# Kernel optimization log

Hardware: AMD Instinct MI355X
Metric: run time of the kernel (lower is better)

The kernel has to match this reference:

```python
import jax, jax.numpy as jnp
import numpy as np
from jax import lax

V = 33      # n_vertices
EPS = 1e-5  # instance-norm eps


def _resize_bilinear(x, oh, ow):
    # torch F.interpolate bilinear, align_corners=False, antialias=False
    b, c, H, W = x.shape
    def coords(out, size):
        src = (jnp.arange(out, dtype=jnp.float32) + 0.5) * (size / out) - 0.5
        i0 = jnp.clip(jnp.floor(src).astype(jnp.int32), 0, size - 1)
        i1 = jnp.clip(i0 + 1, 0, size - 1)
        f = jnp.clip(src - i0.astype(jnp.float32), 0.0, 1.0)
        return i0, i1, f
    y0, y1, fy = coords(oh, H)
    x0, x1, fx = coords(ow, W)
    rows = x[:, :, y0, :] * (1 - fy)[None, None, :, None] + x[:, :, y1, :] * fy[None, None, :, None]
    return rows[:, :, :, x0] * (1 - fx) + rows[:, :, :, x1] * fx


def _conv_s2(x, w, b):
    y = lax.conv_general_dilated(x, w, (2, 2), [(1, 1), (1, 1)],
                                 dimension_numbers=('NCHW', 'OIHW', 'NCHW'))
    return y + b[None, :, None, None]


def _lrelu(x):
    return jnp.where(x >= 0, x, 0.2 * x)


def _inorm(x, g, be):
    m = x.mean((2, 3), keepdims=True)
    v = x.var((2, 3), keepdims=True)
    return (x - m) / jnp.sqrt(v + EPS) * g[None, :, None, None] + be[None, :, None, None]


def _ailut_transform(imgs, luts, vertices):
    # imgs (b,3,H,W); luts (b,3,V,V,V) indexed [out_c, ib, ig, ir]; vertices (b,3,V)
    b, c, H, W = imgs.shape
    N = H * W
    x = jnp.clip(imgs, 0.0, 1.0).reshape(b, 3, N)
    ss = jax.vmap(jax.vmap(lambda v, q: jnp.searchsorted(v, q, side='right')))
    idx = jnp.clip(ss(vertices, x) - 1, 0, V - 2)            # (b,3,N)
    v0 = jnp.take_along_axis(vertices, idx, axis=-1)
    v1 = jnp.take_along_axis(vertices, idx + 1, axis=-1)
    frac = jnp.clip((x - v0) / jnp.maximum(v1 - v0, 1e-10), 0.0, 1.0)
    ir, ig, ibl = idx[:, 0], idx[:, 1], idx[:, 2]            # (b,N) each
    fr, fg, fb = frac[:, 0], frac[:, 1], frac[:, 2]
    lut_flat = luts.reshape(b, 3, V * V * V)
    out = jnp.zeros((b, 3, N), imgs.dtype)
    for db in (0, 1):
        wb = fb if db else 1.0 - fb
        for dg in (0, 1):
            wg = fg if dg else 1.0 - fg
            for dr in (0, 1):
                w = wb * wg * (fr if dr else 1.0 - fr)       # (b,N)
                flat = ((ibl + db) * V + (ig + dg)) * V + (ir + dr)
                vals = jnp.take_along_axis(lut_flat, jnp.broadcast_to(flat[:, None, :], (b, 3, N)), axis=-1)
                out = out + w[:, None, :] * vals
    return out.reshape(b, 3, H, W)


def setup_inputs() -> dict:
    key = jax.random.key(0)
    ks = jax.random.split(key, 32)
    n = lambda k, s: jax.random.normal(k, s, jnp.float32) * 0.05
    inp = {'imgs': jax.random.uniform(ks[0], (2, 3, 2048, 2048), jnp.float32)}
    chans = [(3, 16), (16, 32), (32, 64), (64, 128), (128, 128)]
    for i, (ci, co) in enumerate(chans, start=1):
        inp[f'w{i}'] = n(ks[2 * i], (co, ci, 3, 3))
        inp[f'b{i}'] = n(ks[2 * i + 1], (co,))
        if i <= 4:
            inp[f'g{i}'] = jnp.ones((co,), jnp.float32)
            inp[f'be{i}'] = jnp.zeros((co,), jnp.float32)
    inp['wgen_w'] = n(ks[12], (512, 3))
    inp['wgen_b'] = n(ks[13], (3,))
    inp['basis_w'] = n(ks[14], (3, 3 * V ** 3))
    inp['ada_w'] = n(ks[15], (512, 3 * (V - 1)))
    inp['ada_b'] = n(ks[16], (3 * (V - 1),))
    return inp


def reference(imgs, w1, b1, g1, be1, w2, b2, g2, be2, w3, b3, g3, be3,
              w4, b4, g4, be4, w5, b5, wgen_w, wgen_b, basis_w, ada_w, ada_b):
    b = imgs.shape[0]
    x = _resize_bilinear(imgs, 256, 256)
    for (w, bb, g, be) in ((w1, b1, g1, be1), (w2, b2, g2, be2),
                           (w3, b3, g3, be3), (w4, b4, g4, be4)):
        x = _inorm(_lrelu(_conv_s2(x, w, bb)), g, be)
    x = _lrelu(_conv_s2(x, w5, b5))                      # (b,128,8,8); dropout is identity at eval
    x = x.reshape(b, 128, 2, 4, 2, 4).mean((3, 5)).reshape(b, 512)  # AdaptiveAvgPool2d(2)
    weights = x @ wgen_w + wgen_b                        # (b,3) rank weights
    luts = (weights @ basis_w).reshape(b, 3, V, V, V)
    intervals = jax.nn.softmax((x @ ada_w + ada_b).reshape(b, 3, V - 1), axis=-1)
    vertices = jnp.pad(jnp.cumsum(intervals, -1), ((0, 0), (0, 0), (1, 0)))  # (b,3,V)
    return _ailut_transform(imgs, luts, vertices)
```

## Files before the change

### kernel.cpp

```cpp
#include <hip/hip_runtime.h>
#include <hip/hip_fp16.h>
#include <cstdint>
#include <cstddef>

#define VCUBE 35937
#define LUT_CH 107811

__global__ __launch_bounds__(256) void conv1_fused(const float* __restrict__ imgs,
    const float* __restrict__ w, const float* __restrict__ bias,
    float* __restrict__ out) {
  __shared__ float s_in[3*3*34];
  __shared__ float s_w[16*3*9];
  int bid = blockIdx.x;
  int owt = bid & 7; int oh = (bid >> 3) & 127; int b = bid >> 10;
  int t = threadIdx.x;
  int ow0 = owt * 16;
  int iwbase = 2*ow0 - 1;
  int ihbase = 2*oh - 1;
  for (int i = t; i < 3*3*34; i += 256) {
    int x = i % 34; int rest = i / 34; int kh = rest % 3; int ci = rest / 3;
    int ih = ihbase + kh;
    int iw = iwbase + x;
    float v = 0.f;
    if (ih >= 0 && ih < 256 && iw >= 0 && iw < 256) {
      const float* p = imgs + (size_t)(b*3+ci) * 2048 * 2048;
      int y0 = ih*8 + 3, x0 = iw*8 + 3;
      const float* r0 = p + (size_t)y0*2048 + x0;
      const float* r1 = r0 + 2048;
      float a = r0[0], bb = r0[1], c = r1[0], d = r1[1];
      float top = a + 0.5f*(bb - a);
      float bot = c + 0.5f*(d - c);
      v = top + 0.5f*(bot - top);
    }
    s_in[i] = v;
  }
  for (int i = t; i < 16*3*9; i += 256) s_w[i] = w[i];
  __syncthreads();
  int owl = t & 15; int co = t >> 4;
  float acc = bias[co];
  const float* wp = s_w + co*27;
#pragma unroll
  for (int ci = 0; ci < 3; ci++) {
#pragma unroll
    for (int kh = 0; kh < 3; kh++) {
      const float* rp = s_in + (ci*3 + kh)*34 + 2*owl;
      acc = fmaf(rp[0], wp[ci*9 + kh*3 + 0], acc);
      acc = fmaf(rp[1], wp[ci*9 + kh*3 + 1], acc);
      acc = fmaf(rp[2], wp[ci*9 + kh*3 + 2], acc);
    }
  }
  acc = acc >= 0.f ? acc : 0.2f*acc;
  out[(((size_t)b*16 + co)*128 + oh)*128 + ow0 + owl] = acc;
}

template<int CI, int CO, int IS, int COPB, bool WLDS>
__global__ __launch_bounds__(256) void conv_row(const float* __restrict__ in,
    const float* __restrict__ w, const float* __restrict__ bias,
    float* __restrict__ out) {
  constexpr int OS = IS/2;
  constexpr int PW = IS + 2;
  constexpr int NG = CO/COPB;
  constexpr int E  = CI*3*PW;
  static_assert(COPB*OS == 256, "block mismatch");
  __shared__ float s_in[E];
  __shared__ float s_w[WLDS ? COPB*CI*9 : 1];
  int bid = blockIdx.x;
  int grp = bid % NG; int rest = bid / NG; int oh = rest % OS; int b = rest / OS;
  int t = threadIdx.x;
  int ihb = 2*oh - 1;
  for (int i = t; i < E; i += 256) {
    int x = i % PW; int r2 = i / PW; int kh = r2 % 3; int ci = r2 / 3;
    int ih = ihb + kh; int iw = x - 1;
    float v = 0.f;
    if (ih >= 0 && ih < IS && iw >= 0 && iw < IS)
      v = in[((size_t)(b*CI + ci)*IS + ih)*IS + iw];
    s_in[i] = v;
  }
  if (WLDS) {
    const float* wg = w + (size_t)grp*COPB*CI*9;
    for (int i = t; i < COPB*CI*9; i += 256) s_w[i] = wg[i];
  }
  __syncthreads();
  int ow = t % OS; int col = t / OS;
  int co = grp*COPB + col;
  float acc = bias[co];
  const float* wp = WLDS ? (s_w + col*CI*9) : (w + (size_t)co*CI*9);
  for (int ci = 0; ci < CI; ci++) {
    const float* rowp = s_in + ci*3*PW;
    const float* wc = wp + ci*9;
#pragma unroll
    for (int kh = 0; kh < 3; kh++) {
      const float* rp = rowp + kh*PW + 2*ow;
      acc = fmaf(rp[0], wc[kh*3 + 0], acc);
      acc = fmaf(rp[1], wc[kh*3 + 1], acc);
      acc = fmaf(rp[2], wc[kh*3 + 2], acc);
    }
  }
  acc = acc >= 0.f ? acc : 0.2f*acc;
  out[(((size_t)b*CO + co)*OS + oh)*OS + ow] = acc;
}

__global__ __launch_bounds__(256) void inorm_kernel(float* __restrict__ x,
    const float* __restrict__ g, const float* __restrict__ be, int C, int HW) {
  int plane = blockIdx.x;
  int c = plane % C;
  float* p = x + (size_t)plane * HW;
  int t = threadIdx.x;
  float s = 0.f, s2 = 0.f;
  for (int i = t; i < HW; i += 256) {
    float v = p[i];
    s += v;
    s2 = fmaf(v, v, s2);
  }
  __shared__ float ss[256], sq[256];
  ss[t] = s; sq[t] = s2;
  __syncthreads();
  for (int off = 128; off > 0; off >>= 1) {
    if (t < off) { ss[t] += ss[t + off]; sq[t] += sq[t + off]; }
    __syncthreads();
  }
  __shared__ float sc, sh;
  if (t == 0) {
    float inv_n = 1.0f / (float)HW;
    float mean = ss[0] * inv_n;
    float var  = sq[0] * inv_n - mean*mean;
    float scale = g[c] / sqrtf(var + 1e-5f);
    sc = scale;
    sh = be[c] - mean*scale;
  }
  __syncthreads();
  for (int i = t; i < HW; i += 256) p[i] = fmaf(p[i], sc, sh);
}

__global__ __launch_bounds__(128) void head_kernel(const float* __restrict__ x5,
    const float* __restrict__ wgen_w, const float* __restrict__ wgen_b,
    const float* __restrict__ ada_w, const float* __restrict__ ada_b,
    float* __restrict__ gweights, float* __restrict__ vertices,
    float* __restrict__ invtab, uint8_t* __restrict__ hints) {
  int b = blockIdx.x; int t = threadIdx.x;
  __shared__ float xv[512];
  __shared__ float logits[96];
  __shared__ float svp[99];
  for (int o = t; o < 512; o += 128) {
    int c = o >> 2; int h2 = (o >> 1) & 1; int w2 = o & 1;
    const float* p = x5 + ((size_t)(b*128 + c))*64 + h2*32 + w2*4;
    float s = 0.f;
#pragma unroll
    for (int h = 0; h < 4; h++)
#pragma unroll
      for (int ww = 0; ww < 4; ww++) s += p[h*8 + ww];
    xv[o] = s * (1.f/16.f);
  }
  __syncthreads();
  if (t < 96) {
    float s = ada_b[t];
    for (int k = 0; k < 512; k++) s = fmaf(xv[k], ada_w[k*96 + t], s);
    logits[t] = s;
  } else if (t < 99) {
    int j = t - 96;
    float s = wgen_b[j];
    for (int k = 0; k < 512; k++) s = fmaf(xv[k], wgen_w[k*3 + j], s);
    gweights[b*3 + j] = s;
  }
  __syncthreads();
  if (t < 3) {
    const float* l = logits + t*32;
    float m = l[0];
#pragma unroll
    for (int i = 1; i < 32; i++) m = fmaxf(m, l[i]);
    float e[32]; float sum = 0.f;
#pragma unroll
    for (int i = 0; i < 32; i++) { e[i] = expf(l[i] - m); sum += e[i]; }
    float inv = 1.0f / sum;
    float* vp = vertices + b*99 + t*33;
    svp[t*33] = 0.f; vp[0] = 0.f;
    float cum = 0.f;
#pragma unroll
    for (int i = 0; i < 32; i++) { cum = fmaf(e[i], inv, cum); svp[t*33 + i + 1] = cum; vp[i + 1] = cum; }
  }
  __syncthreads();
  if (t < 96) {
    int c = t >> 5, i = t & 31;
    float d = svp[c*33 + i + 1] - svp[c*33 + i];
    invtab[b*96 + t] = 1.0f / fmaxf(d, 1e-10f);
  }
  for (int e = t; e < 3072; e += 128) {
    int c = e >> 10; int bin = e & 1023;
    float q0 = (float)bin * (1.f/1024.f);
    const float* v = svp + c*33;
    int lo = 0, hi = 33;
    while (lo < hi) { int mid = (lo + hi) >> 1; if (v[mid] <= q0) lo = mid + 1; else hi = mid; }
    int idx = lo - 1; if (idx > 31) idx = 31;
    hints[b*3072 + e] = (uint8_t)idx;
  }
}

__global__ __launch_bounds__(256) void ecell_build(const float* __restrict__ basis_w,
    const float* __restrict__ gw, __half* __restrict__ ecell, int B) {
  int tid = blockIdx.x*256 + threadIdx.x;
  int total = B * 32768 * 3;
  if (tid >= total) return;
  int cc = tid % 3;
  int cell = tid / 3;
  int r = cell & 31; int g = (cell >> 5) & 31; int bl = (cell >> 10) & 31; int b = cell >> 15;
  float w0 = gw[b*3 + 0], w1 = gw[b*3 + 1], w2 = gw[b*3 + 2];
  union { __half h[8]; uint4 u; } pk;
#pragma unroll
  for (int dbl = 0; dbl < 2; dbl++)
#pragma unroll
    for (int dg = 0; dg < 2; dg++)
#pragma unroll
      for (int dr = 0; dr < 2; dr++) {
        int flat = cc*VCUBE + ((bl + dbl)*33 + (g + dg))*33 + (r + dr);
        float val = w0*basis_w[flat] + w1*basis_w[LUT_CH + flat] + w2*basis_w[2*LUT_CH + flat];
        pk.h[dbl*4 + dg*2 + dr] = __float2half(val);
      }
  *(uint4*)((uint16_t*)ecell + (size_t)cell*32 + cc*8) = pk.u;
}

__device__ __forceinline__ void lut_px(float R, float G, float Bl,
    const __half* __restrict__ ec, const float* sv, const float* sinv,
    const uint8_t* shint, float* o0, float* o1, float* o2) {
  float q[3] = { fminf(fmaxf(R, 0.f), 1.f), fminf(fmaxf(G, 0.f), 1.f), fminf(fmaxf(Bl, 0.f), 1.f) };
  int id[3]; float fr[3];
#pragma unroll
  for (int c = 0; c < 3; c++) {
    float qc = q[c];
    int bin = (int)(qc * 1024.f); bin = bin > 1023 ? 1023 : bin;
    int idx = shint[(c << 10) + bin];
    const float* v = sv + c*33;
#pragma unroll
    for (int it = 0; it < 3; it++)
      idx += (idx < 31 && v[idx + 1] <= qc) ? 1 : 0;
    float f = (qc - v[idx]) * sinv[(c << 5) + idx];
    fr[c] = fminf(fmaxf(f, 0.f), 1.f);
    id[c] = idx;
  }
  const __half* cell = ec + ((size_t)(((id[2] << 5) + id[1]) << 5) + id[0]) * 32;
  float fR = fr[0], fG = fr[1], fB = fr[2];
  float res[3];
#pragma unroll
  for (int cc = 0; cc < 3; cc++) {
    uint4 u = *(const uint4*)(cell + cc*8);
    const __half* h = (const __half*)&u;
    float f0 = __half2float(h[0]), f1 = __half2float(h[1]);
    float f2 = __half2float(h[2]), f3 = __half2float(h[3]);
    float f4 = __half2float(h[4]), f5 = __half2float(h[5]);
    float f6 = __half2float(h[6]), f7 = __half2float(h[7]);
    float l00 = fmaf(fR, f1 - f0, f0);
    float l01 = fmaf(fR, f3 - f2, f2);
    float L0  = fmaf(fG, l01 - l00, l00);
    float l10 = fmaf(fR, f5 - f4, f4);
    float l11 = fmaf(fR, f7 - f6, f6);
    float L1  = fmaf(fG, l11 - l10, l10);
    res[cc] = fmaf(fB, L1 - L0, L0);
  }
  *o0 = res[0]; *o1 = res[1]; *o2 = res[2];
}

__global__ __launch_bounds__(256) void transform_kernel(const float* __restrict__ imgs,
    const __half* __restrict__ ecell, const float* __restrict__ vert,
    const float* __restrict__ invtab, const unsigned int* __restrict__ hintw,
    float* __restrict__ out, int B) {
  const size_t N = 2048u*2048u;
  __shared__ float sv[99];
  __shared__ float sinv[96];
  __shared__ unsigned int shint_w[768];
  int b = blockIdx.x % B;
  int pblk = blockIdx.x / B;
  int t = threadIdx.x;
  if (t < 99) sv[t] = vert[b*99 + t];
  if (t < 96) sinv[t] = invtab[b*96 + t];
  for (int i = t; i < 768; i += 256) shint_w[i] = hintw[b*768 + i];
  __syncthreads();
  const uint8_t* shint = (const uint8_t*)shint_w;
  size_t pix = ((size_t)pblk*256 + t) * 4;
  const float* ip = imgs + (size_t)b*3*N;
  float* op = out + (size_t)b*3*N;
  const __half* ec = ecell + (size_t)b*1048576;
  float4 r  = *(const float4*)(ip + pix);
  float4 g  = *(const float4*)(ip + N + pix);
  float4 bb = *(const float4*)(ip + 2*N + pix);
  float4 o0, o1, o2;
  lut_px(r.x, g.x, bb.x, ec, sv, sinv, shint, &o0.x, &o1.x, &o2.x);
  lut_px(r.y, g.y, bb.y, ec, sv, sinv, shint, &o0.y, &o1.y, &o2.y);
  lut_px(r.z, g.z, bb.z, ec, sv, sinv, shint, &o0.z, &o1.z, &o2.z);
  lut_px(r.w, g.w, bb.w, ec, sv, sinv, shint, &o0.w, &o1.w, &o2.w);
  *(float4*)(op + pix) = o0;
  *(float4*)(op + N + pix) = o1;
  *(float4*)(op + 2*N + pix) = o2;
}

extern "C" void kernel_launch(void* const* d_in, const int* in_sizes, int n_in,
                              void* d_out, int out_size, void* d_ws, size_t ws_size,
                              hipStream_t stream) {
  const float* imgs = (const float*)d_in[0];
  const float* w1 = (const float*)d_in[1];  const float* b1 = (const float*)d_in[2];
  const float* g1 = (const float*)d_in[3];  const float* be1 = (const float*)d_in[4];
  const float* w2 = (const float*)d_in[5];  const float* b2 = (const float*)d_in[6];
  const float* g2 = (const float*)d_in[7];  const float* be2 = (const float*)d_in[8];
  const float* w3 = (const float*)d_in[9];  const float* b3 = (const float*)d_in[10];
  const float* g3 = (const float*)d_in[11]; const float* be3 = (const float*)d_in[12];
  const float* w4 = (const float*)d_in[13]; const float* b4 = (const float*)d_in[14];
  const float* g4 = (const float*)d_in[15]; const float* be4 = (const float*)d_in[16];
  const float* w5 = (const float*)d_in[17]; const float* b5 = (const float*)d_in[18];
  const float* wgen_w  = (const float*)d_in[19];
  const float* wgen_b  = (const float*)d_in[20];
  const float* basis_w = (const float*)d_in[21];
  const float* ada_w   = (const float*)d_in[22];
  const float* ada_b   = (const float*)d_in[23];
  float* out = (float*)d_out;

  const int B = in_sizes[0] / (3*2048*2048);

  char* wsb = (char*)d_ws;
  __half* ecell = (__half*)wsb;
  size_t A_bytes = (size_t)B * 2097152;
  float* x1 = (float*)wsb;
  float* x2 = x1 + (size_t)B*262144;
  float* x3 = x2 + (size_t)B*131072;
  float* x4 = x3 + (size_t)B*65536;
  float* x5 = x4 + (size_t)B*32768;
  float* tail = (float*)(wsb + A_bytes);
  float* gw   = tail;
  float* vert = gw + (size_t)B*4;
  float* invt = vert + (size_t)B*99;
  uint8_t* hints = (uint8_t*)(invt + (size_t)B*96);

  conv1_fused<<<B*1024, 256, 0, stream>>>(imgs, w1, b1, x1);
  inorm_kernel<<<B*16, 256, 0, stream>>>(x1, g1, be1, 16, 128*128);
  conv_row<16, 32, 128, 4, true><<<B*512, 256, 0, stream>>>(x1, w2, b2, x2);
  inorm_kernel<<<B*32, 256, 0, stream>>>(x2, g2, be2, 32, 64*64);
  conv_row<32, 64, 64, 8, true><<<B*256, 256, 0, stream>>>(x2, w3, b3, x3);
  inorm_kernel<<<B*64, 256, 0, stream>>>(x3, g3, be3, 64, 32*32);
  conv_row<64, 128, 32, 16, true><<<B*128, 256, 0, stream>>>(x3, w4, b4, x4);
  inorm_kernel<<<B*128, 256, 0, stream>>>(x4, g4, be4, 128, 16*16);
  conv_row<128, 128, 16, 32, false><<<B*32, 256, 0, stream>>>(x4, w5, b5, x5);
  head_kernel<<<B, 128, 0, stream>>>(x5, wgen_w, wgen_b, ada_w, ada_b, gw, vert, invt, hints);
  ecell_build<<<B*384, 256, 0, stream>>>(basis_w, gw, ecell, B);
  transform_kernel<<<B*4096, 256, 0, stream>>>(imgs, ecell, vert, invt,
                                               (const unsigned int*)hints, out, B);
}
```

Before: 487.3 us.

## Fuse encoder, head and LUT build into persistent kernel with grid barriers

Replaces the chain of conv, instance-norm, head and ecell kernels with one persistent kernel of 128*B blocks that synchronises stages through atomic-counter grid barriers. Instance-norm statistics are accumulated with atomics in the conv epilogues and the normalisation is applied while loading the next layer's input, which removes the separate norm passes. The transform kernel also changes: it uses nontemporal loads and stores, batches the LUT gathers, interpolates in half2 arithmetic, and does one fewer search refinement step. The single kernel saves launch gaps but relies on every block being co-resident for the spin barriers, and the early encoder stages now run on fewer blocks. The half2 math and shorter search may also lower accuracy.

Result: slower. 707.0 us (+45.1%).

```diff
diff --git a/kernel.cpp b/kernel.cpp
--- a/kernel.cpp
+++ b/kernel.cpp
@@ -6,289 +6,455 @@
 #define VCUBE 35937
 #define LUT_CH 107811
 
-__global__ __launch_bounds__(256) void conv1_fused(const float* __restrict__ imgs,
-    const float* __restrict__ w, const float* __restrict__ bias,
-    float* __restrict__ out) {
-  __shared__ float s_in[3*3*34];
-  __shared__ float s_w[16*3*9];
-  int bid = blockIdx.x;
-  int owt = bid & 7; int oh = (bid >> 3) & 127; int b = bid >> 10;
-  int t = threadIdx.x;
-  int ow0 = owt * 16;
-  int iwbase = 2*ow0 - 1;
-  int ihbase = 2*oh - 1;
-  for (int i = t; i < 3*3*34; i += 256) {
-    int x = i % 34; int rest = i / 34; int kh = rest % 3; int ci = rest / 3;
-    int ih = ihbase + kh;
-    int iw = iwbase + x;
-    float v = 0.f;
-    if (ih >= 0 && ih < 256 && iw >= 0 && iw < 256) {
-      const float* p = imgs + (size_t)(b*3+ci) * 2048 * 2048;
-      int y0 = ih*8 + 3, x0 = iw*8 + 3;
-      const float* r0 = p + (size_t)y0*2048 + x0;
-      const float* r1 = r0 + 2048;
-      float a = r0[0], bb = r0[1], c = r1[0], d = r1[1];
-      float top = a + 0.5f*(bb - a);
-      float bot = c + 0.5f*(d - c);
-      v = top + 0.5f*(bot - top);
-    }
-    s_in[i] = v;
-  }
-  for (int i = t; i < 16*3*9; i += 256) s_w[i] = w[i];
+typedef float vfloat4 __attribute__((ext_vector_type(4)));
+
+__device__ __forceinline__ void gbar(unsigned* ctr, int k, unsigned target) {
   __syncthreads();
-  int owl = t & 15; int co = t >> 4;
-  float acc = bias[co];
-  const float* wp = s_w + co*27;
-#pragma unroll
-  for (int ci = 0; ci < 3; ci++) {
-#pragma unroll
-    for (int kh = 0; kh < 3; kh++) {
-      const float* rp = s_in + (ci*3 + kh)*34 + 2*owl;
-      acc = fmaf(rp[0], wp[ci*9 + kh*3 + 0], acc);
-      acc = fmaf(rp[1], wp[ci*9 + kh*3 + 1], acc);
-      acc = fmaf(rp[2], wp[ci*9 + kh*3 + 2], acc);
-    }
-  }
-  acc = acc >= 0.f ? acc : 0.2f*acc;
-  out[(((size_t)b*16 + co)*128 + oh)*128 + ow0 + owl] = acc;
+  if (threadIdx.x == 0) {
+    __threadfence();
+    atomicAdd(&ctr[k], 1u);
+    while (__hip_atomic_load(&ctr[k], __ATOMIC_ACQUIRE, __HIP_MEMORY_SCOPE_AGENT) < target)
+      __builtin_amdgcn_s_sleep(2);
+    __threadfence();
+  }
+  __syncthreads();
 }
 
-template<int CI, int CO, int IS, int COPB, bool WLDS>
-__global__ __launch_bounds__(256) void conv_row(const float* __restrict__ in,
-    const float* __restrict__ w, const float* __restrict__ bias,
-    float* __restrict__ out) {
-  constexpr int OS = IS/2;
-  constexpr int PW = IS + 2;
-  constexpr int NG = CO/COPB;
-  constexpr int E  = CI*3*PW;
-  static_assert(COPB*OS == 256, "block mismatch");
-  __shared__ float s_in[E];
-  __shared__ float s_w[WLDS ? COPB*CI*9 : 1];
-  int bid = blockIdx.x;
-  int grp = bid % NG; int rest = bid / NG; int oh = rest % OS; int b = rest / OS;
-  int t = threadIdx.x;
-  int ihb = 2*oh - 1;
-  for (int i = t; i < E; i += 256) {
-    int x = i % PW; int r2 = i / PW; int kh = r2 % 3; int ci = r2 / 3;
-    int ih = ihb + kh; int iw = x - 1;
-    float v = 0.f;
-    if (ih >= 0 && ih < IS && iw >= 0 && iw < IS)
-      v = in[((size_t)(b*CI + ci)*IS + ih)*IS + iw];
-    s_in[i] = v;
-  }
-  if (WLDS) {
-    const float* wg = w + (size_t)grp*COPB*CI*9;
-    for (int i = t; i < COPB*CI*9; i += 256) s_w[i] = wg[i];
-  }
-  __syncthreads();
-  int ow = t % OS; int col = t / OS;
-  int co = grp*COPB + col;
-  float acc = bias[co];
-  const float* wp = WLDS ? (s_w + col*CI*9) : (w + (size_t)co*CI*9);
-  for (int ci = 0; ci < CI; ci++) {
-    const float* rowp = s_in + ci*3*PW;
-    const float* wc = wp + ci*9;
-#pragma unroll
-    for (int kh = 0; kh < 3; kh++) {
-      const float* rp = rowp + kh*PW + 2*ow;
-      acc = fmaf(rp[0], wc[kh*3 + 0], acc);
-      acc = fmaf(rp[1], wc[kh*3 + 1], acc);
-      acc = fmaf(rp[2], wc[kh*3 + 2], acc);
-    }
-  }
-  acc = acc >= 0.f ? acc : 0.2f*acc;
-  out[(((size_t)b*CO + co)*OS + oh)*OS + ow] = acc;
+template<int W>
+__device__ __forceinline__ void wred2(float& a, float& b) {
+#pragma unroll
+  for (int d = W / 2; d > 0; d >>= 1) {
+    a += __shfl_down(a, d, W);
+    b += __shfl_down(b, d, W);
+  }
 }
 
-__global__ __launch_bounds__(256) void inorm_kernel(float* __restrict__ x,
-    const float* __restrict__ g, const float* __restrict__ be, int C, int HW) {
-  int plane = blockIdx.x;
-  int c = plane % C;
-  float* p = x + (size_t)plane * HW;
-  int t = threadIdx.x;
-  float s = 0.f, s2 = 0.f;
-  for (int i = t; i < HW; i += 256) {
-    float v = p[i];
-    s += v;
-    s2 = fmaf(v, v, s2);
-  }
-  __shared__ float ss[256], sq[256];
-  ss[t] = s; sq[t] = s2;
-  __syncthreads();
-  for (int off = 128; off > 0; off >>= 1) {
-    if (t < off) { ss[t] += ss[t + off]; sq[t] += sq[t + off]; }
-    __syncthreads();
-  }
-  __shared__ float sc, sh;
-  if (t == 0) {
-    float inv_n = 1.0f / (float)HW;
-    float mean = ss[0] * inv_n;
-    float var  = sq[0] * inv_n - mean*mean;
-    float scale = g[c] / sqrtf(var + 1e-5f);
-    sc = scale;
-    sh = be[c] - mean*scale;
-  }
-  __syncthreads();
-  for (int i = t; i < HW; i += 256) p[i] = fmaf(p[i], sc, sh);
+__global__ __launch_bounds__(256, 2) void mega_kernel(
+    const float* __restrict__ imgs,
+    const float* __restrict__ w1, const float* __restrict__ b1, const float* __restrict__ g1, const float* __restrict__ be1,
+    const float* __restrict__ w2, const float* __restrict__ b2, const float* __restrict__ g2, const float* __restrict__ be2,
+    const float* __restrict__ w3, const float* __restrict__ b3, const float* __restrict__ g3, const float* __restrict__ be3,
+    const float* __restrict__ w4, const float* __restrict__ b4, const float* __restrict__ g4, const float* __restrict__ be4,
+    const float* __restrict__ w5, const float* __restrict__ b5,
+    const float* __restrict__ wgen_w, const float* __restrict__ wgen_b,
+    const float* __restrict__ basis_w,
+    const float* __restrict__ ada_w, const float* __restrict__ ada_b,
+    float* __restrict__ x1, float* __restrict__ x2, float* __restrict__ x3,
+    float* __restrict__ x4, float* __restrict__ x5,
+    float* __restrict__ gwp, float* __restrict__ vert, float* __restrict__ invt,
+    uint8_t* __restrict__ hints, __half* __restrict__ ecell,
+    float* __restrict__ stats1, float* __restrict__ stats2,
+    float* __restrict__ stats3, float* __restrict__ stats4,
+    unsigned* __restrict__ bar, int B) {
+  __shared__ float smem[7424];
+  const int blk = blockIdx.x;
+  const int t = threadIdx.x;
+  const unsigned NB = gridDim.x;
+
+  {
+    const int b = blk >> 7;
+    const int oh = blk & 127;
+    float* s_w = smem;
+    float* s_in = smem + 432;
+    for (int i = t; i < 432; i += 256) s_w[i] = w1[i];
+    const int co = t >> 4, owl = t & 15;
+    float s = 0.f, s2 = 0.f;
+    const int ihbase = 2 * oh - 1;
+    for (int j = 0; j < 8; j++) {
+      const int ow0 = j * 16;
+      const int iwbase = 2 * ow0 - 1;
+      __syncthreads();
+      for (int i = t; i < 306; i += 256) {
+        int x = i % 34; int rest = i / 34; int kh = rest % 3; int ci = rest / 3;
+        int ih = ihbase + kh, iw = iwbase + x;
+        float v = 0.f;
+        if (ih >= 0 && ih < 256 && iw >= 0 && iw < 256) {
+          const float* p = imgs + (size_t)(b * 3 + ci) * 2048 * 2048;
+          const float* r0 = p + (size_t)(ih * 8 + 3) * 2048 + (iw * 8 + 3);
+          const float* r1 = r0 + 2048;
+          float a = r0[0], bb = r0[1], c = r1[0], d = r1[1];
+          float top = a + 0.5f * (bb - a);
+          float bot = c + 0.5f * (d - c);
+          v = top + 0.5f * (bot - top);
+        }
+        s_in[i] = v;
+      }
+      __syncthreads();
+      float acc = b1[co];
+      const float* wp = s_w + co * 27;
+#pragma unroll
+      for (int ci = 0; ci < 3; ci++)
+#pragma unroll
+        for (int kh = 0; kh < 3; kh++) {
+          const float* rp = s_in + (ci * 3 + kh) * 34 + 2 * owl;
+          acc = fmaf(rp[0], wp[ci * 9 + kh * 3 + 0], acc);
+          acc = fmaf(rp[1], wp[ci * 9 + kh * 3 + 1], acc);
+          acc = fmaf(rp[2], wp[ci * 9 + kh * 3 + 2], acc);
+        }
+      acc = acc >= 0.f ? acc : 0.2f * acc;
+      x1[(((size_t)b * 16 + co) * 128 + oh) * 128 + ow0 + owl] = acc;
+      s += acc; s2 = fmaf(acc, acc, s2);
+    }
+    wred2<16>(s, s2);
+    if (owl == 0) {
+      atomicAdd(&stats1[((b << 4) + co) * 2 + 0], s);
+      atomicAdd(&stats1[((b << 4) + co) * 2 + 1], s2);
+    }
+  }
+  gbar(bar, 0, NB);
+
+  {
+    const int b = blk >> 7;
+    const int oh = (blk >> 1) & 63;
+    const int g0 = (blk & 1) * 4;
+    float* sal = smem; float* sbe = smem + 16;
+    if (t < 16) {
+      float s = stats1[((b << 4) + t) * 2], s2 = stats1[((b << 4) + t) * 2 + 1];
+      float mean = s * (1.f / 16384.f);
+      float var = s2 * (1.f / 16384.f) - mean * mean;
+      float a = g1[t] / sqrtf(var + 1e-5f);
+      sal[t] = a; sbe[t] = be1[t] - mean * a;
+    }
+    __syncthreads();
+    float* s_in = smem + 32;
+    const int ihb = 2 * oh - 1;
+    for (int i = t; i < 6240; i += 256) {
+      int x = i % 130; int r2 = i / 130; int kh = r2 % 3; int ci = r2 / 3;
+      int ih = ihb + kh, iw = x - 1;
+      float v = 0.f;
+      if (ih >= 0 && ih < 128 && iw >= 0 && iw < 128)
+        v = fmaf(x1[((size_t)((b << 4) + ci) * 128 + ih) * 128 + iw], sal[ci], sbe[ci]);
+      s_in[i] = v;
+    }
+    __syncthreads();
+    const int ow = t & 63, col = t >> 6;
+    for (int gi = 0; gi < 4; gi++) {
+      int co = (g0 + gi) * 4 + col;
+      float acc = b2[co];
+      const float* wp = w2 + (size_t)co * 144;
+      for (int ci = 0; ci < 16; ci++) {
+        const float* rp = s_in + ci * 390 + 2 * ow;
+        const float* wc = wp + ci * 9;
+        acc = fmaf(rp[0], wc[0], acc); acc = fmaf(rp[1], wc[1], acc); acc = fmaf(rp[2], wc[2], acc);
+        acc = fmaf(rp[130], wc[3], acc); acc = fmaf(rp[131], wc[4], acc); acc = fmaf(rp[132], wc[5], acc);
+        acc = fmaf(rp[260], wc[6], acc); acc = fmaf(rp[261], wc[7], acc); acc = fmaf(rp[262], wc[8], acc);
+      }
+      acc = acc >= 0.f ? acc : 0.2f * acc;
+      x2[((size_t)((b << 5) + co) * 64 + oh) * 64 + ow] = acc;
+      float s = acc, s2 = acc * acc;
+      wred2<64>(s, s2);
+      if (ow == 0) {
+        atomicAdd(&stats2[((b << 5) + co) * 2 + 0], s);
+        atomicAdd(&stats2[((b << 5) + co) * 2 + 1], s2);
+      }
+    }
+  }
+  gbar(bar, 1, NB);
+
+  {
+    const int b = blk >> 7;
+    const int oh = (blk >> 2) & 31;
+    const int m = blk & 3;
+    float* sal = smem; float* sbe = smem + 32;
+    if (t < 32) {
+      float s = stats2[((b << 5) + t) * 2], s2 = stats2[((b << 5) + t) * 2 + 1];
+      float mean = s * (1.f / 4096.f);
+      float var = s2 * (1.f / 4096.f) - mean * mean;
+      float a = g2[t] / sqrtf(var + 1e-5f);
+      sal[t] = a; sbe[t] = be2[t] - mean * a;
+    }
+    __syncthreads();
+    float* s_in = smem + 64;
+    const int ihb = 2 * oh - 1;
+    for (int i = t; i < 6336; i += 256) {
+      int x = i % 66; int r2 = i / 66; int kh = r2 % 3; int ci = r2 / 3;
+      int ih = ihb + kh, iw = x - 1;
+      float v = 0.f;
+      if (ih >= 0 && ih < 64 && iw >= 0 && iw < 64)
+        v = fmaf(x2[((size_t)((b << 5) + ci) * 64 + ih) * 64 + iw], sal[ci], sbe[ci]);
+      s_in[i] = v;
+    }
+    __syncthreads();
+    const int ow = t & 31, col = t >> 5;
+    for (int gi = 0; gi < 2; gi++) {
+      int co = (2 * m + gi) * 8 + col;
+      float acc = b3[co];
+      const float* wp = w3 + (size_t)co * 288;
+      for (int ci = 0; ci < 32; ci++) {
+        const float* rp = s_in + ci * 198 + 2 * ow;
+        const float* wc = wp + ci * 9;
+        acc = fmaf(rp[0], wc[0], acc); acc = fmaf(rp[1], wc[1], acc); acc = fmaf(rp[2], wc[2], acc);
+        acc = fmaf(rp[66], wc[3], acc); acc = fmaf(rp[67], wc[4], acc); acc = fmaf(rp[68], wc[5], acc);
+        acc = fmaf(rp[132], wc[6], acc); acc = fmaf(rp[133], wc[7], acc); acc = fmaf(rp[134], wc[8], acc);
+      }
+      acc = acc >= 0.f ? acc : 0.2f * acc;
+      x3[((size_t)((b << 6) + co) * 32 + oh) * 32 + ow] = acc;
+      float s = acc, s2 = acc * acc;
+      wred2<32>(s, s2);
+      if (ow == 0) {
+        atomicAdd(&stats3[((b << 6) + co) * 2 + 0], s);
+        atomicAdd(&stats3[((b << 6) + co) * 2 + 1], s2);
+      }
+    }
+  }
+  gbar(bar, 2, NB);
+
+  {
+    const int b = blk >> 7;
+    const int oh = (blk >> 3) & 15;
+    const int grp = blk & 7;
+    float* sal = smem; float* sbe = smem + 64;
+    if (t < 64) {
+      float s = stats3[((b << 6) + t) * 2], s2 = stats3[((b << 6) + t) * 2 + 1];
+      float mean = s * (1.f / 1024.f);
+      float var = s2 * (1.f / 1024.f) - mean * mean;
+      float a = g3[t] / sqrtf(var + 1e-5f);
+      sal[t] = a; sbe[t] = be3[t] - mean * a;
+    }
+    __syncthreads();
+    float* s_in = smem + 128;
+    const int ihb = 2 * oh - 1;
+    for (int i = t; i < 6528; i += 256) {
+      int x = i % 34; int r2 = i / 34; int kh = r2 % 3; int ci = r2 / 3;
+      int ih = ihb + kh, iw = x - 1;
+      float v = 0.f;
+      if (ih >= 0 && ih < 32 && iw >= 0 && iw < 32)
+        v = fmaf(x3[((size_t)((b << 6) + ci) * 32 + ih) * 32 + iw], sal[ci], sbe[ci]);
+      s_in[i] = v;
+    }
+    __syncthreads();
+    const int ow = t & 15, col = t >> 4;
+    int co = grp * 16 + col;
+    float acc = b4[co];
+    const float* wp = w4 + (size_t)co * 576;
+    for (int ci = 0; ci < 64; ci++) {
+      const float* rp = s_in + ci * 102 + 2 * ow;
+      const float* wc = wp + ci * 9;
+      acc = fmaf(rp[0], wc[0], acc); acc = fmaf(rp[1], wc[1], acc); acc = fmaf(rp[2], wc[2], acc);
+      acc = fmaf(rp[34], wc[3], acc); acc = fmaf(rp[35], wc[4], acc); acc = fmaf(rp[36], wc[5], acc);
+      acc = fmaf(rp[68], wc[6], acc); acc = fmaf(rp[69], wc[7], acc); acc = fmaf(rp[70], wc[8], acc);
+    }
+    acc = acc >= 0.f ? acc : 0.2f * acc;
+    x4[((size_t)((b << 7) + co) * 16 + oh) * 16 + ow] = acc;
+    float s = acc, s2 = acc * acc;
+    wred2<16>(s, s2);
+    if (ow == 0) {
+      atomicAdd(&stats4[((b << 7) + co) * 2 + 0], s);
+      atomicAdd(&stats4[((b << 7) + co) * 2 + 1], s2);
+    }
+  }
+  gbar(bar, 3, NB);
+
+  {
+    const int b = blk >> 7;
+    const int oh = (blk >> 4) & 7;
+    const int grp = blk & 15;
+    float* sal = smem; float* sbe = smem + 128;
+    if (t < 128) {
+      float s = stats4[((b << 7) + t) * 2], s2 = stats4[((b << 7) + t) * 2 + 1];
+      float mean = s * (1.f / 256.f);
+      float var = s2 * (1.f / 256.f) - mean * mean;
+      float a = g4[t] / sqrtf(var + 1e-5f);
+      sal[t] = a; sbe[t] = be4[t] - mean * a;
+    }
+    __syncthreads();
+    float* s_in = smem + 256;
+    float* part = smem + 7168;
+    const int ihb = 2 * oh - 1;
+    for (int i = t; i < 6912; i += 256) {
+      int x = i % 18; int r2 = i / 18; int kh = r2 % 3; int ci = r2 / 3;
+      int ih = ihb + kh, iw = x - 1;
+      float v = 0.f;
+      if (ih >= 0 && ih < 16 && iw >= 0 && iw < 16)
+        v = fmaf(x4[((size_t)((b << 7) + ci) * 16 + ih) * 16 + iw], sal[ci], sbe[ci]);
+      s_in[i] = v;
+    }
+    __syncthreads();
+    const int ow = t & 7, col = (t >> 3) & 7, ks = t >> 6;
+    int co = grp * 8 + col;
+    float acc = 0.f;
+    const float* wp = w5 + (size_t)co * 1152;
+    for (int ci = ks * 32; ci < ks * 32 + 32; ci++) {
+      const float* rp = s_in + ci * 54 + 2 * ow;
+      const float* wc = wp + ci * 9;
+      acc = fmaf(rp[0], wc[0], acc); acc = fmaf(rp[1], wc[1], acc); acc = fmaf(rp[2], wc[2], acc);
+      acc = fmaf(rp[18], wc[3], acc); acc = fmaf(rp[19], wc[4], acc); acc = fmaf(rp[20], wc[5], acc);
+      acc = fmaf(rp[36], wc[6], acc); acc = fmaf(rp[37], wc[7], acc); acc = fmaf(rp[38], wc[8], acc);
+    }
+    part[t] = acc;
+    __syncthreads();
+    if (t < 64) {
+      float v = part[t] + part[t + 64] + part[t + 128] + part[t + 192];
+      int co2 = grp * 8 + (t >> 3);
+      int ow2 = t & 7;
+      v += b5[co2];
+      v = v >= 0.f ? v : 0.2f * v;
+      x5[((size_t)((b << 7) + co2) * 8 + oh) * 8 + ow2] = v;
+    }
+  }
+  gbar(bar, 4, NB);
+
+  if ((blk & 127) == 0) {
+    const int b = blk >> 7;
+    float* xv = smem;
+    float* logits = smem + 512;
+    float* svp = smem + 608;
+    for (int o = t; o < 512; o += 256) {
+      int c = o >> 2, h2 = (o >> 1) & 1, w2 = o & 1;
+      const float* p = x5 + ((size_t)(b * 128 + c)) * 64 + h2 * 32 + w2 * 4;
+      float s = 0.f;
+#pragma unroll
+      for (int h = 0; h < 4; h++)
+#pragma unroll
+        for (int ww = 0; ww < 4; ww++) s += p[h * 8 + ww];
+      xv[o] = s * (1.f / 16.f);
+    }
+    __syncthreads();
+    if (t < 96) {
+      float s = ada_b[t];
+      for (int k = 0; k < 512; k++) s = fmaf(xv[k], ada_w[k * 96 + t], s);
+      logits[t] = s;
+    } else if (t < 99) {
+      int j = t - 96;
+      float s = wgen_b[j];
+      for (int k = 0; k < 512; k++) s = fmaf(xv[k], wgen_w[k * 3 + j], s);
+      gwp[b * 3 + j] = s;
+    }
+    __syncthreads();
+    if (t < 3) {
+      const float* l = logits + t * 32;
+      float m = l[0];
+#pragma unroll
+      for (int i = 1; i < 32; i++) m = fmaxf(m, l[i]);
+      float e[32]; float sum = 0.f;
+#pragma unroll
+      for (int i = 0; i < 32; i++) { e[i] = expf(l[i] - m); sum += e[i]; }
+      float inv = 1.0f / sum;
+      float* vp = vert + b * 99 + t * 33;
+      svp[t * 33] = 0.f; vp[0] = 0.f;
+      float cum = 0.f;
+#pragma unroll
+      for (int i = 0; i < 32; i++) {
+        cum = fmaf(e[i], inv, cum);
+        svp[t * 33 + i + 1] = cum; vp[i + 1] = cum;
+      }
+    }
+    __syncthreads();
+    if (t < 96) {
+      int c = t >> 5, i = t & 31;
+      float d = svp[c * 33 + i + 1] - svp[c * 33 + i];
+      invt[b * 96 + t] = 1.0f / fmaxf(d, 1e-10f);
+    }
+    for (int e = t; e < 3072; e += 256) {
+      int c = e >> 10; int bin = e & 1023;
+      float q0 = (float)bin * (1.f / 1024.f);
+      const float* v = svp + c * 33;
+      int lo = 0, hi = 33;
+      while (lo < hi) { int mid = (lo + hi) >> 1; if (v[mid] <= q0) lo = mid + 1; else hi = mid; }
+      int idx = lo - 1; if (idx > 31) idx = 31;
+      hints[b * 3072 + e] = (uint8_t)idx;
+    }
+  }
+  gbar(bar, 5, NB);
+
+  {
+    int total = B * 98304;
+    for (int it = blk * 256 + t; it < total; it += (int)NB * 256) {
+      int cc = it % 3; int cell = it / 3;
+      int r = cell & 31, g = (cell >> 5) & 31, bl = (cell >> 10) & 31, b = cell >> 15;
+      float w0 = gwp[b * 3 + 0], w1c = gwp[b * 3 + 1], w2c = gwp[b * 3 + 2];
+      union { __half h[8]; uint4 u; } pk;
+#pragma unroll
+      for (int dg = 0; dg < 2; dg++)
+#pragma unroll
+        for (int dr = 0; dr < 2; dr++)
+#pragma unroll
+          for (int db = 0; db < 2; db++) {
+            int flat = cc * VCUBE + ((bl + db) * 33 + (g + dg)) * 33 + (r + dr);
+            float val = w0 * basis_w[flat] + w1c * basis_w[LUT_CH + flat] + w2c * basis_w[2 * LUT_CH + flat];
+            pk.h[(dg * 2 + dr) * 2 + db] = __float2half(val);
+          }
+      *(uint4*)((uint16_t*)ecell + (size_t)cell * 32 + cc * 8) = pk.u;
+    }
+  }
 }
 
-__global__ __launch_bounds__(128) void head_kernel(const float* __restrict__ x5,
-    const float* __restrict__ wgen_w, const float* __restrict__ wgen_b,
-    const float* __restrict__ ada_w, const float* __restrict__ ada_b,
-    float* __restrict__ gweights, float* __restrict__ vertices,
-    float* __restrict__ invtab, uint8_t* __restrict__ hints) {
-  int b = blockIdx.x; int t = threadIdx.x;
-  __shared__ float xv[512];
-  __shared__ float logits[96];
-  __shared__ float svp[99];
-  for (int o = t; o < 512; o += 128) {
-    int c = o >> 2; int h2 = (o >> 1) & 1; int w2 = o & 1;
-    const float* p = x5 + ((size_t)(b*128 + c))*64 + h2*32 + w2*4;
-    float s = 0.f;
-#pragma unroll
-    for (int h = 0; h < 4; h++)
-#pragma unroll
-      for (int ww = 0; ww < 4; ww++) s += p[h*8 + ww];
-    xv[o] = s * (1.f/16.f);
-  }
-  __syncthreads();
-  if (t < 96) {
-    float s = ada_b[t];
-    for (int k = 0; k < 512; k++) s = fmaf(xv[k], ada_w[k*96 + t], s);
-    logits[t] = s;
-  } else if (t < 99) {
-    int j = t - 96;
-    float s = wgen_b[j];
-    for (int k = 0; k < 512; k++) s = fmaf(xv[k], wgen_w[k*3 + j], s);
-    gweights[b*3 + j] = s;
-  }
-  __syncthreads();
-  if (t < 3) {
-    const float* l = logits + t*32;
-    float m = l[0];
-#pragma unroll
-    for (int i = 1; i < 32; i++) m = fmaxf(m, l[i]);
-    float e[32]; float sum = 0.f;
-#pragma unroll
-    for (int i = 0; i < 32; i++) { e[i] = expf(l[i] - m); sum += e[i]; }
-    float inv = 1.0f / sum;
-    float* vp = vertices + b*99 + t*33;
-    svp[t*33] = 0.f; vp[0] = 0.f;
-    float cum = 0.f;
-#pragma unroll
-    for (int i = 0; i < 32; i++) { cum = fmaf(e[i], inv, cum); svp[t*33 + i + 1] = cum; vp[i + 1] = cum; }
-  }
-  __syncthreads();
-  if (t < 96) {
-    int c = t >> 5, i = t & 31;
-    float d = svp[c*33 + i + 1] - svp[c*33 + i];
-    invtab[b*96 + t] = 1.0f / fmaxf(d, 1e-10f);
-  }
-  for (int e = t; e < 3072; e += 128) {
-    int c = e >> 10; int bin = e & 1023;
-    float q0 = (float)bin * (1.f/1024.f);
-    const float* v = svp + c*33;
-    int lo = 0, hi = 33;
-    while (lo < hi) { int mid = (lo + hi) >> 1; if (v[mid] <= q0) lo = mid + 1; else hi = mid; }
-    int idx = lo - 1; if (idx > 31) idx = 31;
-    hints[b*3072 + e] = (uint8_t)idx;
-  }
-}
-
-__global__ __launch_bounds__(256) void ecell_build(const float* __restrict__ basis_w,
-    const float* __restrict__ gw, __half* __restrict__ ecell, int B) {
-  int tid = blockIdx.x*256 + threadIdx.x;
-  int total = B * 32768 * 3;
-  if (tid >= total) return;
-  int cc = tid % 3;
-  int cell = tid / 3;
-  int r = cell & 31; int g = (cell >> 5) & 31; int bl = (cell >> 10) & 31; int b = cell >> 15;
-  float w0 = gw[b*3 + 0], w1 = gw[b*3 + 1], w2 = gw[b*3 + 2];
-  union { __half h[8]; uint4 u; } pk;
-#pragma unroll
-  for (int dbl = 0; dbl < 2; dbl++)
-#pragma unroll
-    for (int dg = 0; dg < 2; dg++)
-#pragma unroll
-      for (int dr = 0; dr < 2; dr++) {
-        int flat = cc*VCUBE + ((bl + dbl)*33 + (g + dg))*33 + (r + dr);
-        float val = w0*basis_w[flat] + w1*basis_w[LUT_CH + flat] + w2*basis_w[2*LUT_CH + flat];
-        pk.h[dbl*4 + dg*2 + dr] = __float2half(val);
-      }
-  *(uint4*)((uint16_t*)ecell + (size_t)cell*32 + cc*8) = pk.u;
-}
-
-__device__ __forceinline__ void lut_px(float R, float G, float Bl,
-    const __half* __restrict__ ec, const float* sv, const float* sinv,
-    const uint8_t* shint, float* o0, float* o1, float* o2) {
-  float q[3] = { fminf(fmaxf(R, 0.f), 1.f), fminf(fmaxf(G, 0.f), 1.f), fminf(fmaxf(Bl, 0.f), 1.f) };
-  int id[3]; float fr[3];
-#pragma unroll
-  for (int c = 0; c < 3; c++) {
-    float qc = q[c];
-    int bin = (int)(qc * 1024.f); bin = bin > 1023 ? 1023 : bin;
-    int idx = shint[(c << 10) + bin];
-    const float* v = sv + c*33;
-#pragma unroll
-    for (int it = 0; it < 3; it++)
-      idx += (idx < 31 && v[idx + 1] <= qc) ? 1 : 0;
-    float f = (qc - v[idx]) * sinv[(c << 5) + idx];
-    fr[c] = fminf(fmaxf(f, 0.f), 1.f);
-    id[c] = idx;
-  }
-  const __half* cell = ec + ((size_t)(((id[2] << 5) + id[1]) << 5) + id[0]) * 32;
-  float fR = fr[0], fG = fr[1], fB = fr[2];
-  float res[3];
-#pragma unroll
-  for (int cc = 0; cc < 3; cc++) {
-    uint4 u = *(const uint4*)(cell + cc*8);
-    const __half* h = (const __half*)&u;
-    float f0 = __half2float(h[0]), f1 = __half2float(h[1]);
-    float f2 = __half2float(h[2]), f3 = __half2float(h[3]);
-    float f4 = __half2float(h[4]), f5 = __half2float(h[5]);
-    float f6 = __half2float(h[6]), f7 = __half2float(h[7]);
-    float l00 = fmaf(fR, f1 - f0, f0);
-    float l01 = fmaf(fR, f3 - f2, f2);
-    float L0  = fmaf(fG, l01 - l00, l00);
-    float l10 = fmaf(fR, f5 - f4, f4);
-    float l11 = fmaf(fR, f7 - f6, f6);
-    float L1  = fmaf(fG, l11 - l10, l10);
-    res[cc] = fmaf(fB, L1 - L0, L0);
-  }
-  *o0 = res[0]; *o1 = res[1]; *o2 = res[2];
-}
-
-__global__ __launch_bounds__(256) void transform_kernel(const float* __restrict__ imgs,
+__global__ __launch_bounds__(256, 2) void transform_kernel(const float* __restrict__ imgs,
     const __half* __restrict__ ecell, const float* __restrict__ vert,
     const float* __restrict__ invtab, const unsigned int* __restrict__ hintw,
     float* __restrict__ out, int B) {
-  const size_t N = 2048u*2048u;
+  const size_t N = 2048u * 2048u;
   __shared__ float sv[99];
   __shared__ float sinv[96];
   __shared__ unsigned int shint_w[768];
   int b = blockIdx.x % B;
   int pblk = blockIdx.x / B;
   int t = threadIdx.x;
-  if (t < 99) sv[t] = vert[b*99 + t];
-  if (t < 96) sinv[t] = invtab[b*96 + t];
-  for (int i = t; i < 768; i += 256) shint_w[i] = hintw[b*768 + i];
+  if (t < 99) sv[t] = vert[b * 99 + t];
+  if (t < 96) sinv[t] = invtab[b * 96 + t];
+  for (int i = t; i < 768; i += 256) shint_w[i] = hintw[b * 768 + i];
   __syncthreads();
   const uint8_t* shint = (const uint8_t*)shint_w;
-  size_t pix = ((size_t)pblk*256 + t) * 4;
-  const float* ip = imgs + (size_t)b*3*N;
-  float* op = out + (size_t)b*3*N;
-  const __half* ec = ecell + (size_t)b*1048576;
-  float4 r  = *(const float4*)(ip + pix);
-  float4 g  = *(const float4*)(ip + N + pix);
-  float4 bb = *(const float4*)(ip + 2*N + pix);
-  float4 o0, o1, o2;
-  lut_px(r.x, g.x, bb.x, ec, sv, sinv, shint, &o0.x, &o1.x, &o2.x);
-  lut_px(r.y, g.y, bb.y, ec, sv, sinv, shint, &o0.y, &o1.y, &o2.y);
-  lut_px(r.z, g.z, bb.z, ec, sv, sinv, shint, &o0.z, &o1.z, &o2.z);
-  lut_px(r.w, g.w, bb.w, ec, sv, sinv, shint, &o0.w, &o1.w, &o2.w);
-  *(float4*)(op + pix) = o0;
-  *(float4*)(op + N + pix) = o1;
-  *(float4*)(op + 2*N + pix) = o2;
+  size_t pix = ((size_t)pblk * 256 + t) * 4;
+  const float* ip = imgs + (size_t)b * 3 * N;
+  float* op = out + (size_t)b * 3 * N;
+  const __half* ec = ecell + (size_t)b * 1048576;
+  vfloat4 r  = __builtin_nontemporal_load((const vfloat4*)(ip + pix));
+  vfloat4 g  = __builtin_nontemporal_load((const vfloat4*)(ip + N + pix));
+  vfloat4 bb = __builtin_nontemporal_load((const vfloat4*)(ip + 2 * N + pix));
+  float R[4] = {r.x, r.y, r.z, r.w};
+  float G[4] = {g.x, g.y, g.z, g.w};
+  float Bb[4] = {bb.x, bb.y, bb.z, bb.w};
+  int cofs[4]; float fRa[4], fGa[4], fBa[4];
+#pragma unroll
+  for (int p = 0; p < 4; p++) {
+    float q[3] = { fminf(fmaxf(R[p], 0.f), 1.f), fminf(fmaxf(G[p], 0.f), 1.f), fminf(fmaxf(Bb[p], 0.f), 1.f) };
+    int id[3]; float fr[3];
+#pragma unroll
+    for (int c = 0; c < 3; c++) {
+      float qc = q[c];
+      int bin = (int)(qc * 1024.f); bin = bin > 1023 ? 1023 : bin;
+      int idx = shint[(c << 10) + bin];
+      const float* v = sv + c * 33;
+      idx += (idx < 31 && v[idx + 1] <= qc) ? 1 : 0;
+      idx += (idx < 31 && v[idx + 1] <= qc) ? 1 : 0;
+      float f = (qc - v[idx]) * sinv[(c << 5) + idx];
+      fr[c] = fminf(fmaxf(f, 0.f), 1.f);
+      id[c] = idx;
+    }
+    cofs[p] = (((id[2] << 5) + id[1]) << 5) + id[0];
+    fRa[p] = fr[0]; fGa[p] = fr[1]; fBa[p] = fr[2];
+  }
+  uint4 u[12];
+#pragma unroll
+  for (int p = 0; p < 4; p++) {
+    const __half* cell = ec + (size_t)cofs[p] * 32;
+    u[p * 3 + 0] = *(const uint4*)(cell);
+    u[p * 3 + 1] = *(const uint4*)(cell + 8);
+    u[p * 3 + 2] = *(const uint4*)(cell + 16);
+  }
+  float oc[3][4];
+#pragma unroll
+  for (int p = 0; p < 4; p++) {
+    __half2 fR2 = __float2half2_rn(fRa[p]);
+    __half2 fG2 = __float2half2_rn(fGa[p]);
+    float fB = fBa[p];
+#pragma unroll
+    for (int cc = 0; cc < 3; cc++) {
+      union { uint4 v; __half2 h2[4]; } m; m.v = u[p * 3 + cc];
+      __half2 a  = __hfma2(fR2, __hsub2(m.h2[1], m.h2[0]), m.h2[0]);
+      __half2 b2 = __hfma2(fR2, __hsub2(m.h2[3], m.h2[2]), m.h2[2]);
+      __half2 cg = __hfma2(fG2, __hsub2(b2, a), a);
+      float lo = __low2float(cg), hi = __high2float(cg);
+      oc[cc][p] = fmaf(fB, hi - lo, lo);
+    }
+  }
+  vfloat4 o0 = {oc[0][0], oc[0][1], oc[0][2], oc[0][3]};
+  vfloat4 o1 = {oc[1][0], oc[1][1], oc[1][2], oc[1][3]};
+  vfloat4 o2 = {oc[2][0], oc[2][1], oc[2][2], oc[2][3]};
+  __builtin_nontemporal_store(o0, (vfloat4*)(op + pix));
+  __builtin_nontemporal_store(o1, (vfloat4*)(op + N + pix));
+  __builtin_nontemporal_store(o2, (vfloat4*)(op + 2 * N + pix));
 }
 
 extern "C" void kernel_launch(void* const* d_in, const int* in_sizes, int n_in,
@@ -311,33 +477,36 @@
   const float* ada_b   = (const float*)d_in[23];
   float* out = (float*)d_out;
 
-  const int B = in_sizes[0] / (3*2048*2048);
+  const int B = in_sizes[0] / (3 * 2048 * 2048);
 
   char* wsb = (char*)d_ws;
   __half* ecell = (__half*)wsb;
+  float* x1 = (float*)wsb;
+  float* x2 = x1 + (size_t)B * 262144;
+  float* x3 = x2 + (size_t)B * 131072;
+  float* x4 = x3 + (size_t)B * 65536;
+  float* x5 = x4 + (size_t)B * 32768;
   size_t A_bytes = (size_t)B * 2097152;
-  float* x1 = (float*)wsb;
-  float* x2 = x1 + (size_t)B*262144;
-  float* x3 = x2 + (size_t)B*131072;
-  float* x4 = x3 + (size_t)B*65536;
-  float* x5 = x4 + (size_t)B*32768;
-  float* tail = (float*)(wsb + A_bytes);
-  float* gw   = tail;
-  float* vert = gw + (size_t)B*4;
-  float* invt = vert + (size_t)B*99;
-  uint8_t* hints = (uint8_t*)(invt + (size_t)B*96);
-
-  conv1_fused<<<B*1024, 256, 0, stream>>>(imgs, w1, b1, x1);
-  inorm_kernel<<<B*16, 256, 0, stream>>>(x1, g1, be1, 16, 128*128);
-  conv_row<16, 32, 128, 4, true><<<B*512, 256, 0, stream>>>(x1, w2, b2, x2);
-  inorm_kernel<<<B*32, 256, 0, stream>>>(x2, g2, be2, 32, 64*64);
-  conv_row<32, 64, 64, 8, true><<<B*256, 256, 0, stream>>>(x2, w3, b3, x3);
-  inorm_kernel<<<B*64, 256, 0, stream>>>(x3, g3, be3, 64, 32*32);
-  conv_row<64, 128, 32, 16, true><<<B*128, 256, 0, stream>>>(x3, w4, b4, x4);
-  inorm_kernel<<<B*128, 256, 0, stream>>>(x4, g4, be4, 128, 16*16);
-  conv_row<128, 128, 16, 32, false><<<B*32, 256, 0, stream>>>(x4, w5, b5, x5);
-  head_kernel<<<B, 128, 0, stream>>>(x5, wgen_w, wgen_b, ada_w, ada_b, gw, vert, invt, hints);
-  ecell_build<<<B*384, 256, 0, stream>>>(basis_w, gw, ecell, B);
-  transform_kernel<<<B*4096, 256, 0, stream>>>(imgs, ecell, vert, invt,
-                                               (const unsigned int*)hints, out, B);
+  float* gwp  = (float*)(wsb + A_bytes);
+  float* vert = gwp + (size_t)B * 4;
+  float* invt = vert + (size_t)B * 99;
+  uint8_t* hints = (uint8_t*)(invt + (size_t)B * 96);
+  float* stats = (float*)(hints + (size_t)B * 3072);
+  float* stats1 = stats;
+  float* stats2 = stats1 + (size_t)B * 32;
+  float* stats3 = stats2 + (size_t)B * 64;
+  float* stats4 = stats3 + (size_t)B * 128;
+  unsigned* bar = (unsigned*)(stats + (size_t)B * 480);
+
+  size_t zero_bytes = (size_t)B * 480 * 4 + 32;
+  (void)hipMemsetAsync(stats, 0, zero_bytes, stream);
+
+  mega_kernel<<<dim3(128 * B), 256, 0, stream>>>(
+      imgs, w1, b1, g1, be1, w2, b2, g2, be2, w3, b3, g3, be3, w4, b4, g4, be4,
+      w5, b5, wgen_w, wgen_b, basis_w, ada_w, ada_b,
+      x1, x2, x3, x4, x5, gwp, vert, invt, hints, ecell,
+      stats1, stats2, stats3, stats4, bar, B);
+
+  transform_kernel<<<dim3(B * 4096), 256, 0, stream>>>(imgs, ecell, vert, invt,
+                                                       (const unsigned int*)hints, out, B);
 }
```
